# Kernel optimization log

Measured on AMD Instinct MI355X. Metric: run time of the kernel, lower is better.

The kernel has to match this reference:

```python
import jax, jax.numpy as jnp
import numpy as np

W_MAX, STEP, LEAK = 8, 1, 2
KSIZE = (W_MAX - 1) * (STEP + LEAK)  # 21
THETA = 40          # dense * w_max // 2 = 10*8//2
FODEP = KSIZE       # 21
PAD = KSIZE         # 21
NEURONS = 512


def make_w_kernel_table():
    # StepFireLeak response table, shape [w_max, KSIZE], time-flipped like torch .flip(1)
    w = np.arange(W_MAX, dtype=np.float64)[:, None]
    t = np.arange(KSIZE, dtype=np.float64)[None, :]
    w_step = np.maximum(np.floor(1.0 + t / STEP), 0.0)
    w_leak = np.maximum(np.ceil(w + ((w - 1.0) * STEP - t) / LEAK), 0.0)
    table = np.minimum(w_step, w_leak).astype(np.int32)[:, ::-1]
    return jnp.asarray(table)


def setup_inputs() -> dict:
    key = jax.random.key(0)
    k1, k2 = jax.random.split(key)
    B, C, S, T = 64, 1, 784, 500
    # sparse binary spike trains, p ~ 0.05
    input_spikes = (jax.random.randint(k1, (B, C, S, T), 0, 20) == 0).astype(jnp.float32)
    # learned integer synaptic weights in [0, w_max-1]
    weight = jax.random.randint(k2, (NEURONS, C * S), 0, W_MAX, dtype=jnp.int32)
    return {
        "input_spikes": input_spikes,
        "weight": weight,
        "w_kernel_table": make_w_kernel_table(),
    }


def reference(input_spikes, weight, w_kernel_table):
    B, C, S, T = input_spikes.shape
    x = input_spikes.reshape(B, C * S, T)
    # gather per-weight response kernel: [neurons, C*S, KSIZE]
    kernel = w_kernel_table[weight].astype(x.dtype)
    # cross-correlation, same semantics as torch conv1d (kernel already flipped)
    pot = jax.lax.conv_general_dilated(
        x, kernel, window_strides=(1,), padding=[(PAD, PAD)],
        dimension_numbers=("NCH", "OIH", "NCH"))
    pot = pot.reshape(B, 1, NEURONS, -1)            # [B, out_ch, neurons, Tp]
    pot_tfirst = jnp.moveaxis(pot, -1, 0)           # [Tp, B, ch, neurons]

    def step(depression, p_t):
        # p_t: [B, ch, neurons]
        winner = jnp.argmax(p_t, axis=-1)           # [B, ch]
        maxv = jnp.max(p_t, axis=-1)
        cond = (maxv > THETA) & (depression == 0)   # min_depression is all zeros
        winners_t = jax.nn.one_hot(winner, NEURONS, dtype=p_t.dtype) \
            * cond[..., None].astype(p_t.dtype)
        depression = jnp.maximum(0, depression + cond.astype(jnp.int32) * (FODEP + 1) - 1)
        return depression, winners_t

    dep0 = jnp.zeros((B, 1), jnp.int32)
    _, winners = jax.lax.scan(step, dep0, pot_tfirst)   # [Tp, B, ch, neurons]
    return jnp.moveaxis(winners, 0, -1)                 # [B, ch, neurons, Tp]
```

## Files before the change

kernel.cpp:

```cpp
#include <hip/hip_runtime.h>
#include <stdint.h>

#define NEURONS 512
#define SYN     784
#define TIN     500
#define TP      522
#define TPAD    528
#define BATCH   64
#define NCOL    (BATCH*TPAD)
#define XW2     18
#define NKK     98

typedef int i32x4 __attribute__((ext_vector_type(4)));

__global__ __launch_bounds__(256) void k_prep(
    const int* __restrict__ w, uint2* __restrict__ apk,
    const float* __restrict__ x, uint32_t* __restrict__ xbT,
    unsigned long long* __restrict__ partial)
{
    __shared__ unsigned char nib[16][128];
    const int bid = blockIdx.x, tid = threadIdx.x;
    if (bid < 1568) {
        int u = bid * 256 + tid;
        int half = u & 1, m = (u >> 1) & 15, quad = (u >> 5) & 3;
        int rowblk = (u >> 7) & 31, kk = u >> 12;
        int n = rowblk * 16 + m;
        int s = kk * 8 + quad * 2 + half;
        int wv = w[n * SYN + s];
        uint2 v;
        v.x = (wv < 4)  ? (1u << (8 * wv))       : 0u;
        v.y = (wv >= 4) ? (1u << (8 * (wv - 4))) : 0u;
        apk[u] = v;
        if (u < NCOL) partial[u] = 0ull;
    } else {
        int r0 = (bid - 1568) * 16;
        for (int e = tid; e < 2048; e += 256) {
            int row = e >> 7, q4 = e & 127;
            unsigned char v = 0;
            if (q4 < 125) {
                float4 f = *(const float4*)(x + (size_t)(r0 + row) * TIN + q4 * 4);
                v = (unsigned char)((f.x != 0.f) | ((f.y != 0.f) << 1) |
                                    ((f.z != 0.f) << 2) | ((f.w != 0.f) << 3));
            }
            nib[row][q4] = v;
        }
        __syncthreads();
        int row = tid >> 4, d = tid & 15;
        uint64_t u = *(const uint64_t*)&nib[row][d * 8];
        uint32_t wd = 0;
#pragma unroll
        for (int q = 0; q < 8; ++q)
            wd |= ((uint32_t)((u >> (8 * q)) & 0xFull)) << (4 * q);
        if (d == 15) wd &= 0xFFFFFu;
        int grow = r0 + row;
        int b = grow / SYN, s = grow - b * SYN;
        xbT[(size_t)(b * XW2 + 1 + d) * SYN + s] = wd;
        if (d == 0) {
            xbT[(size_t)(b * XW2) * SYN + s] = 0u;
            xbT[(size_t)(b * XW2 + 17) * SYN + s] = 0u;
        }
    }
}

__global__ __launch_bounds__(256) void k_bbuild(
    const uint32_t* __restrict__ xbT,
    const int*      __restrict__ wk,
    uint4*          __restrict__ Bg)
{
    __shared__ uint2 T0[2048];
    __shared__ uint2 T1[1024];
    __shared__ uint2 tapv[21];

    const int tid = threadIdx.x;
    if (tid < 21) {
        uint32_t lo = 0, hi = 0;
        for (int q = 0; q < 4; ++q) {
            lo |= ((uint32_t)wk[q * 21 + tid]) << (8 * q);
            hi |= ((uint32_t)wk[(q + 4) * 21 + tid]) << (8 * q);
        }
        tapv[tid] = make_uint2(lo, hi);
    }
    __syncthreads();
    for (int e = tid; e < 3072; e += 256) {
        int base_t = (e < 2048) ? 0 : 11;
        uint32_t mm = (e < 2048) ? e : (e - 2048);
        uint2 a = make_uint2(0u, 0u);
        while (mm) {
            int p = __builtin_ctz(mm);
            uint2 tv = tapv[base_t + p];
            a.x += tv.x; a.y += tv.y;
            mm &= mm - 1;
        }
        if (e < 2048) T0[e] = a; else T1[e - 2048] = a;
    }

    const int col = blockIdx.x * 64 + (tid >> 2);
    const int sp  = tid & 3;
    int b  = col / TPAD, t = col - b * TPAD;
    int bp = t + 11;
    const uint32_t xbase = (uint32_t)((b * XW2 + (bp >> 5)) * SYN + sp * 2);
    const uint32_t xsh   = (uint32_t)(bp & 31);
    __syncthreads();

    const int kk0 = blockIdx.y * 49, kk1 = kk0 + 49;
    for (int kk = kk0; kk < kk1; ++kk) {
        const uint2* px = (const uint2*)(xbT + xbase + kk * 8);
        uint2 lo = px[0];
        uint2 hi = px[SYN / 2];
        uint32_t w0 = __builtin_amdgcn_alignbit(hi.x, lo.x, xsh) & 0x1FFFFFu;
        uint32_t w1 = __builtin_amdgcn_alignbit(hi.y, lo.y, xsh) & 0x1FFFFFu;
        uint32_t l0 = w0 & 2047u, h0 = w0 >> 11;
        uint32_t l1 = w1 & 2047u, h1 = w1 >> 11;
        uint2 a0 = make_uint2(0u, 0u), a1 = make_uint2(0u, 0u);
        if (l0) { uint2 u = T0[l0]; a0.x += u.x; a0.y += u.y; }
        if (h0) { uint2 v = T1[h0]; a0.x += v.x; a0.y += v.y; }
        if (l1) { uint2 u = T0[l1]; a1.x += u.x; a1.y += u.y; }
        if (h1) { uint2 v = T1[h1]; a1.x += v.x; a1.y += v.y; }
        Bg[(size_t)(kk * NCOL + col) * 4 + sp] = make_uint4(a0.x, a0.y, a1.x, a1.y);
    }
}

__global__ __launch_bounds__(256, 4) void k_gemm2(
    const i32x4* __restrict__ Apk4,
    const i32x4* __restrict__ Bg4,
    unsigned long long* __restrict__ partial)
{
    __shared__ unsigned long long red[128 * 4];

    const int tid  = threadIdx.x;
    const int lane = tid & 63;
    const int wn   = tid >> 6;
    const int quad = lane >> 4, l15 = lane & 15;

    const int phys   = blockIdx.x;
    const int xcd    = phys & 7;
    const int jb     = phys >> 3;
    const int colblk = xcd * 33 + (jb >> 2);
    const int rowblk = jb & 3;

    const int m0   = rowblk * 128;
    const int col0 = colblk * 128;
    const int rb0  = rowblk * 8;
    const int cb   = col0 + wn * 32 + l15;

    const uint32_t pa0 = (uint32_t)(rb0 * 64 + lane);
    const uint32_t pb0 = (uint32_t)(cb * 4 + quad);

    i32x4 acc[8][2];
#pragma unroll
    for (int i = 0; i < 8; ++i)
#pragma unroll
        for (int jj = 0; jj < 2; ++jj) { i32x4 z = {0, 0, 0, 0}; acc[i][jj] = z; }

    for (int kk = 0; kk < NKK; ++kk) {
        i32x4 bf0 = Bg4[pb0 + (uint32_t)kk * (NCOL * 4)];
        i32x4 bf1 = Bg4[pb0 + (uint32_t)kk * (NCOL * 4) + 64];
        i32x4 af[8];
#pragma unroll
        for (int i = 0; i < 8; ++i)
            af[i] = Apk4[pa0 + (uint32_t)kk * 2048 + i * 64];
#pragma unroll
        for (int i = 0; i < 8; ++i) {
            acc[i][0] = __builtin_amdgcn_mfma_i32_16x16x64_i8(af[i], bf0, acc[i][0], 0, 0, 0);
            acc[i][1] = __builtin_amdgcn_mfma_i32_16x16x64_i8(af[i], bf1, acc[i][1], 0, 0, 0);
        }
    }

#pragma unroll
    for (int jj = 0; jj < 2; ++jj) {
        unsigned long long bp = 0ull;
#pragma unroll
        for (int i = 0; i < 8; ++i)
#pragma unroll
            for (int r = 0; r < 4; ++r) {
                int grow = m0 + i * 16 + quad * 4 + r;
                unsigned long long pk =
                    (((unsigned long long)(uint32_t)acc[i][jj][r]) << 32) |
                    (unsigned long long)(uint32_t)(511 - grow);
                bp = pk > bp ? pk : bp;
            }
        red[(wn * 32 + jj * 16 + l15) * 4 + quad] = bp;
    }
    __syncthreads();
    if (tid < 128) {
        unsigned long long b = red[tid * 4];
#pragma unroll
        for (int u = 1; u < 4; ++u) {
            unsigned long long v = red[tid * 4 + u];
            b = v > b ? v : b;
        }
        atomicMax(&partial[col0 + tid], b);
    }
}

__global__ __launch_bounds__(256) void k_firescan(
    const unsigned long long* __restrict__ partial, float* __restrict__ out)
{
    __shared__ int argL[576];
    __shared__ unsigned long long fm[9];
    const int b = blockIdx.x, tid = threadIdx.x;
    const int lane = tid & 63, wv = tid >> 6;

    float4* ob = (float4*)(out + (size_t)b * (NEURONS * TP));
    for (int i = tid; i < (NEURONS * TP) / 4; i += 256)
        ob[i] = make_float4(0.f, 0.f, 0.f, 0.f);

#pragma unroll
    for (int p = 0; p < 3; ++p) {
        int chunk = p * 4 + wv;
        if (chunk < 9) {
            int t = chunk * 64 + lane;
            int col = b * TPAD + (t < TPAD ? t : TPAD - 1);
            unsigned long long pv = partial[col];
            int best = (int)(pv >> 32);
            argL[t] = 511 - (int)(pv & 0xFFFFFFFFull);
            unsigned long long f = __ballot((t < TP) && (best > 40));
            if (lane == 0) fm[chunk] = f;
        }
    }
    __syncthreads();

    if (tid == 0) {
        unsigned short ts[26];
        int nf = 0, dep = 0;
        for (int c = 0; c < 9; ++c) {
            unsigned long long mm = fm[c];
            int pos = 0;
            while (pos < 64) {
                if (dep > 0) {
                    int adv = dep < (64 - pos) ? dep : (64 - pos);
                    dep -= adv; pos += adv; mm >>= adv;
                    continue;
                }
                if (mm == 0) break;
                int z = __builtin_ctzll(mm);
                pos += z; mm >>= z;
                ts[nf++] = (unsigned short)(c * 64 + pos);
                dep = 21; ++pos; mm >>= 1;
            }
        }
        for (int i = 0; i < nf; ++i) {
            int t = ts[i];
            out[(size_t)b * (NEURONS * TP) + (size_t)argL[t] * TP + t] = 1.0f;
        }
    }
}

__global__ __launch_bounds__(256) void k_gemm_fused(
    const i32x4*    __restrict__ Apk4,
    const uint32_t* __restrict__ xbT,
    const int*      __restrict__ wk,
    unsigned long long* __restrict__ partial)
{
    __shared__ uint2 T0[2048];
    __shared__ uint2 T1[1024];
    __shared__ unsigned long long red[128 * 4];
    __shared__ uint2 tapv[21];

    const int tid  = threadIdx.x;
    const int lane = tid & 63;
    const int wn   = tid >> 6;
    const int quad = lane >> 4, l15 = lane & 15;
    const int m0   = blockIdx.x * 128;
    const int col0 = blockIdx.y * 128;
    const int rb0  = blockIdx.x * 8;

    if (tid < 21) {
        uint32_t lo = 0, hi = 0;
        for (int q = 0; q < 4; ++q) {
            lo |= ((uint32_t)wk[q * 21 + tid]) << (8 * q);
            hi |= ((uint32_t)wk[(q + 4) * 21 + tid]) << (8 * q);
        }
        tapv[tid] = make_uint2(lo, hi);
    }
    __syncthreads();
    for (int e = tid; e < 3072; e += 256) {
        int base_t = (e < 2048) ? 0 : 11;
        uint32_t mm = (e < 2048) ? e : (e - 2048);
        uint2 a = make_uint2(0u, 0u);
        while (mm) {
            int p = __builtin_ctz(mm);
            uint2 tv = tapv[base_t + p];
            a.x += tv.x; a.y += tv.y;
            mm &= mm - 1;
        }
        if (e < 2048) T0[e] = a; else T1[e - 2048] = a;
    }

    uint32_t base[2]; uint32_t sh[2];
#pragma unroll
    for (int j = 0; j < 2; ++j) {
        int c = col0 + wn * 32 + j * 16 + l15;
        int b = c / TPAD, t = c - b * TPAD;
        int bp = t + 11;
        base[j] = (uint32_t)((b * XW2 + (bp >> 5)) * SYN + quad * 2);
        sh[j]   = (uint32_t)(bp & 31);
    }
    __syncthreads();

    i32x4 acc[8][2];
#pragma unroll
    for (int i = 0; i < 8; ++i)
#pragma unroll
        for (int j = 0; j < 2; ++j) { i32x4 z = {0, 0, 0, 0}; acc[i][j] = z; }

    for (int kk = 0; kk < NKK; ++kk) {
        i32x4 af[8];
#pragma unroll
        for (int i = 0; i < 8; ++i)
            af[i] = Apk4[(size_t)(kk * 32 + rb0 + i) * 64 + lane];
        i32x4 bf[2];
#pragma unroll
        for (int j = 0; j < 2; ++j) {
            const uint2* px = (const uint2*)(xbT + base[j] + kk * 8);
            uint2 lo = px[0];
            uint2 hi = px[SYN / 2];
            uint32_t win0 = __builtin_amdgcn_alignbit(hi.x, lo.x, sh[j]) & 0x1FFFFFu;
            uint32_t win1 = __builtin_amdgcn_alignbit(hi.y, lo.y, sh[j]) & 0x1FFFFFu;
            uint2 u0 = T0[win0 & 2047], v0 = T1[win0 >> 11];
            uint2 u1 = T0[win1 & 2047], v1 = T1[win1 >> 11];
            i32x4 bb;
            bb[0] = (int)(u0.x + v0.x); bb[1] = (int)(u0.y + v0.y);
            bb[2] = (int)(u1.x + v1.x); bb[3] = (int)(u1.y + v1.y);
            bf[j] = bb;
        }
#pragma unroll
        for (int i = 0; i < 8; ++i)
#pragma unroll
            for (int j = 0; j < 2; ++j)
                acc[i][j] = __builtin_amdgcn_mfma_i32_16x16x64_i8(af[i], bf[j], acc[i][j], 0, 0, 0);
    }

#pragma unroll
    for (int j = 0; j < 2; ++j) {
        unsigned long long bp = 0ull;
#pragma unroll
        for (int i = 0; i < 8; ++i)
#pragma unroll
            for (int r = 0; r < 4; ++r) {
                int grow = m0 + i * 16 + quad * 4 + r;
                unsigned long long pk =
                    (((unsigned long long)(uint32_t)acc[i][j][r]) << 32) |
                    (unsigned long long)(uint32_t)(511 - grow);
                bp = pk > bp ? pk : bp;
            }
        red[(wn * 32 + j * 16 + l15) * 4 + quad] = bp;
    }
    __syncthreads();
    if (tid < 128) {
        unsigned long long b = red[tid * 4];
#pragma unroll
        for (int u = 1; u < 4; ++u) {
            unsigned long long v = red[tid * 4 + u];
            b = v > b ? v : b;
        }
        atomicMax(&partial[col0 + tid], b);
    }
}

__global__ void k_fire(const unsigned long long* __restrict__ partial,
                       int* __restrict__ argT, unsigned long long* __restrict__ fireM) {
    int id   = blockIdx.x * 4 + (threadIdx.x >> 6);
    int lane = threadIdx.x & 63;
    int b    = id / 9, ch = id - b * 9;
    int t    = ch * 64 + lane;
    int col  = b * TPAD + (t < TPAD ? t : TPAD - 1);
    unsigned long long pv = partial[col];
    int best = (int)(pv >> 32);
    int arg  = 511 - (int)(pv & 0xFFFFFFFFull);
    argT[id * 64 + lane] = arg;
    unsigned long long f = __ballot((t < TP) && (best > 40));
    if (lane == 0) fireM[id] = f;
}

__global__ void k_scan(const unsigned long long* __restrict__ fireM,
                       const int* __restrict__ argT, float* __restrict__ out) {
    int b = threadIdx.x;
    unsigned long long fm[9];
#pragma unroll
    for (int c = 0; c < 9; ++c) fm[c] = fireM[b * 9 + c];
    unsigned short ts[26];
    int nf = 0, dep = 0;
    for (int c = 0; c < 9; ++c) {
        unsigned long long mm = fm[c];
        int pos = 0;
        while (pos < 64) {
            if (dep > 0) {
                int adv = dep < (64 - pos) ? dep : (64 - pos);
                dep -= adv; pos += adv; mm >>= adv;
                continue;
            }
            if (mm == 0) break;
            int z = __builtin_ctzll(mm);
            pos += z; mm >>= z;
            ts[nf++] = (unsigned short)(c * 64 + pos);
            dep = 21; ++pos; mm >>= 1;
        }
    }
    for (int i = 0; i < nf; ++i) {
        int t = ts[i];
        int a = argT[(b * 9 + (t >> 6)) * 64 + (t & 63)];
        out[(size_t)b * (NEURONS * TP) + (size_t)a * TP + t] = 1.0f;
    }
}

extern "C" void kernel_launch(void* const* d_in, const int* in_sizes, int n_in,
                              void* d_out, int out_size, void* d_ws, size_t ws_size,
                              hipStream_t stream) {
    const float* x      = (const float*)d_in[0];
    const int*   weight = (const int*)d_in[1];
    const int*   wk     = (const int*)d_in[2];

    char* ws = (char*)d_ws;
    uint2*              Apk     = (uint2*)(ws);
    uint32_t*           xbT     = (uint32_t*)(ws + 3211264);
    unsigned long long* partial = (unsigned long long*)(ws + 6823936);
    int*                argT    = (int*)(ws + 7094272);
    unsigned long long* fireM   = (unsigned long long*)(ws + 7241728);
    uint4*              Bg      = (uint4*)(ws + 7246336);
    const size_t WS_SPLIT_NEED = 7246336ull + 211746816ull;

    float* out = (float*)d_out;

    if (ws_size >= WS_SPLIT_NEED) {
        k_prep<<<4704, 256, 0, stream>>>(weight, Apk, x, xbT, partial);
        k_bbuild<<<dim3(528, 2), 256, 0, stream>>>(xbT, wk, Bg);
        k_gemm2<<<1056, 256, 0, stream>>>((const i32x4*)Apk, (const i32x4*)Bg, partial);
        k_firescan<<<BATCH, 256, 0, stream>>>(partial, out);
    } else {
        hipMemsetAsync(out, 0, (size_t)out_size * 4, stream);
        hipMemsetAsync(partial, 0, NCOL * 8, stream);
        k_prep<<<4704, 256, 0, stream>>>(weight, Apk, x, xbT, partial);
        k_gemm_fused<<<dim3(4, NCOL / 128), 256, 0, stream>>>((const i32x4*)Apk, xbT, wk, partial);
        k_fire<<<144, 256, 0, stream>>>(partial, argT, fireM);
        k_scan<<<1, 64, 0, stream>>>(fireM, argT, out);
    }
}
```

Baseline: 403.0 us.

## Fuse prep, GEMM with on-the-fly B build, and fire scan into one cooperative kernel

Replaces the four-kernel pipeline with a single persistent cooperative kernel that uses grid syncs between phases. The GEMM now builds B fragments on the fly from the bit-packed spike table and LDS lookup tables, instead of staging a large precomputed B matrix in global memory. The output zeroing moves from the fire-scan phase into the prep phase. Together these remove launch overhead and the large B write and re-read. The cost is extra ALU and LDS work inside the GEMM loop, grid-sync latency, and possible occupancy limits from the larger combined shared-memory footprint.

Measured after the change: 702.7 us. +74.4%, slower.

```diff
diff --git a/kernel.cpp b/kernel.cpp
--- a/kernel.cpp
+++ b/kernel.cpp
@@ -1,5 +1,8 @@
 #include <hip/hip_runtime.h>
+#include <hip/hip_cooperative_groups.h>
 #include <stdint.h>
+
+namespace cg = cooperative_groups;
 
 #define NEURONS 512
 #define SYN     784
@@ -10,13 +13,241 @@
 #define NCOL    (BATCH*TPAD)
 #define XW2     18
 #define NKK     98
+#define OUTF4   ((BATCH*NEURONS*TP)/4)
 
 typedef int i32x4 __attribute__((ext_vector_type(4)));
+
+__global__ __launch_bounds__(256, 4) void k_all(
+    const int* __restrict__ w, uint2* __restrict__ apk,
+    const float* __restrict__ x, uint32_t* __restrict__ xbT,
+    unsigned long long* __restrict__ partial, float* __restrict__ out,
+    const int* __restrict__ wk)
+{
+    __shared__ unsigned char nib[16][128];
+    __shared__ uint2 T0[2048];
+    __shared__ uint2 T1[1024];
+    __shared__ unsigned long long red[128 * 4];
+    __shared__ uint2 tapv[21];
+    __shared__ int argL[576];
+    __shared__ unsigned long long fm[9];
+
+    cg::grid_group grid = cg::this_grid();
+    const int tid = threadIdx.x;
+
+    for (int vb = blockIdx.x; vb < 5216; vb += gridDim.x) {
+        if (vb < 1568) {
+            int u = vb * 256 + tid;
+            int half = u & 1, m = (u >> 1) & 15, quad = (u >> 5) & 3;
+            int rowblk = (u >> 7) & 31, kk = u >> 12;
+            int n = rowblk * 16 + m;
+            int s = kk * 8 + quad * 2 + half;
+            int wv = w[n * SYN + s];
+            uint2 v;
+            v.x = (wv < 4)  ? (1u << (8 * wv))       : 0u;
+            v.y = (wv >= 4) ? (1u << (8 * (wv - 4))) : 0u;
+            apk[u] = v;
+            if (u < NCOL) partial[u] = 0ull;
+        } else if (vb < 4704) {
+            int r0 = (vb - 1568) * 16;
+            __syncthreads();
+            for (int e = tid; e < 2048; e += 256) {
+                int row = e >> 7, q4 = e & 127;
+                unsigned char v = 0;
+                if (q4 < 125) {
+                    float4 f = *(const float4*)(x + (size_t)(r0 + row) * TIN + q4 * 4);
+                    v = (unsigned char)((f.x != 0.f) | ((f.y != 0.f) << 1) |
+                                        ((f.z != 0.f) << 2) | ((f.w != 0.f) << 3));
+                }
+                nib[row][q4] = v;
+            }
+            __syncthreads();
+            int row = tid >> 4, d = tid & 15;
+            uint64_t u = *(const uint64_t*)&nib[row][d * 8];
+            uint32_t wd = 0;
+#pragma unroll
+            for (int q = 0; q < 8; ++q)
+                wd |= ((uint32_t)((u >> (8 * q)) & 0xFull)) << (4 * q);
+            if (d == 15) wd &= 0xFFFFFu;
+            int grow = r0 + row;
+            int b = grow / SYN, s = grow - b * SYN;
+            xbT[(size_t)(b * XW2 + 1 + d) * SYN + s] = wd;
+            if (d == 0) {
+                xbT[(size_t)(b * XW2) * SYN + s] = 0u;
+                xbT[(size_t)(b * XW2 + 17) * SYN + s] = 0u;
+            }
+        } else {
+            const float4 z = make_float4(0.f, 0.f, 0.f, 0.f);
+            float4* out4 = (float4*)out;
+            for (size_t i = (size_t)(vb - 4704) * 256 + tid; i < OUTF4; i += 512 * 256)
+                out4[i] = z;
+        }
+    }
+    grid.sync();
+
+    const int lane = tid & 63;
+    const int wn   = tid >> 6;
+    const int quad = lane >> 4, l15 = lane & 15;
+
+    if (tid < 21) {
+        uint32_t lo = 0, hi = 0;
+        for (int q = 0; q < 4; ++q) {
+            lo |= ((uint32_t)wk[q * 21 + tid]) << (8 * q);
+            hi |= ((uint32_t)wk[(q + 4) * 21 + tid]) << (8 * q);
+        }
+        tapv[tid] = make_uint2(lo, hi);
+    }
+    __syncthreads();
+    for (int e = tid; e < 3072; e += 256) {
+        int base_t = (e < 2048) ? 0 : 11;
+        uint32_t mm = (e < 2048) ? e : (e - 2048);
+        uint2 a = make_uint2(0u, 0u);
+        while (mm) {
+            int p = __builtin_ctz(mm);
+            uint2 tv = tapv[base_t + p];
+            a.x += tv.x; a.y += tv.y;
+            mm &= mm - 1;
+        }
+        if (e < 2048) T0[e] = a; else T1[e - 2048] = a;
+    }
+    __syncthreads();
+
+    for (int vb = blockIdx.x; vb < 1056; vb += gridDim.x) {
+        const int xcd    = vb & 7;
+        const int jb     = vb >> 3;
+        const int colblk = xcd * 33 + (jb >> 2);
+        const int rowblk = jb & 3;
+
+        const int m0   = rowblk * 128;
+        const int col0 = colblk * 128;
+        const int rb0  = rowblk * 8;
+
+        uint32_t base[2]; uint32_t sh[2];
+#pragma unroll
+        for (int j = 0; j < 2; ++j) {
+            int c = col0 + wn * 32 + j * 16 + l15;
+            int b = c / TPAD, t = c - b * TPAD;
+            int bp = t + 11;
+            base[j] = (uint32_t)((b * XW2 + (bp >> 5)) * SYN + quad * 2);
+            sh[j]   = (uint32_t)(bp & 31);
+        }
+        const uint32_t pa0 = (uint32_t)(rb0 * 64 + lane);
+
+        i32x4 acc[8][2];
+#pragma unroll
+        for (int i = 0; i < 8; ++i)
+#pragma unroll
+            for (int j = 0; j < 2; ++j) { i32x4 z = {0, 0, 0, 0}; acc[i][j] = z; }
+
+        const i32x4* Apk4 = (const i32x4*)apk;
+        for (int kk = 0; kk < NKK; ++kk) {
+            i32x4 af[8];
+#pragma unroll
+            for (int i = 0; i < 8; ++i)
+                af[i] = Apk4[pa0 + (uint32_t)kk * 2048 + i * 64];
+            i32x4 bf[2];
+#pragma unroll
+            for (int j = 0; j < 2; ++j) {
+                const uint2* px = (const uint2*)(xbT + base[j] + kk * 8);
+                uint2 lo = px[0];
+                uint2 hi = px[SYN / 2];
+                uint32_t win0 = __builtin_amdgcn_alignbit(hi.x, lo.x, sh[j]) & 0x1FFFFFu;
+                uint32_t win1 = __builtin_amdgcn_alignbit(hi.y, lo.y, sh[j]) & 0x1FFFFFu;
+                uint32_t l0 = win0 & 2047u, h0 = win0 >> 11;
+                uint32_t l1 = win1 & 2047u, h1 = win1 >> 11;
+                uint2 a0 = make_uint2(0u, 0u), a1 = make_uint2(0u, 0u);
+                if (l0) { uint2 u = T0[l0]; a0.x += u.x; a0.y += u.y; }
+                if (h0) { uint2 v = T1[h0]; a0.x += v.x; a0.y += v.y; }
+                if (l1) { uint2 u = T0[l1]; a1.x += u.x; a1.y += u.y; }
+                if (h1) { uint2 v = T1[h1]; a1.x += v.x; a1.y += v.y; }
+                i32x4 bb;
+                bb[0] = (int)a0.x; bb[1] = (int)a0.y;
+                bb[2] = (int)a1.x; bb[3] = (int)a1.y;
+                bf[j] = bb;
+            }
+#pragma unroll
+            for (int i = 0; i < 8; ++i)
+#pragma unroll
+                for (int j = 0; j < 2; ++j)
+                    acc[i][j] = __builtin_amdgcn_mfma_i32_16x16x64_i8(af[i], bf[j], acc[i][j], 0, 0, 0);
+        }
+
+#pragma unroll
+        for (int j = 0; j < 2; ++j) {
+            unsigned long long bp = 0ull;
+#pragma unroll
+            for (int i = 0; i < 8; ++i)
+#pragma unroll
+                for (int r = 0; r < 4; ++r) {
+                    int grow = m0 + i * 16 + quad * 4 + r;
+                    unsigned long long pk =
+                        (((unsigned long long)(uint32_t)acc[i][j][r]) << 32) |
+                        (unsigned long long)(uint32_t)(511 - grow);
+                    bp = pk > bp ? pk : bp;
+                }
+            red[(wn * 32 + j * 16 + l15) * 4 + quad] = bp;
+        }
+        __syncthreads();
+        if (tid < 128) {
+            unsigned long long b = red[tid * 4];
+#pragma unroll
+            for (int u = 1; u < 4; ++u) {
+                unsigned long long v = red[tid * 4 + u];
+                b = v > b ? v : b;
+            }
+            atomicMax(&partial[col0 + tid], b);
+        }
+        __syncthreads();
+    }
+    grid.sync();
+
+    if (blockIdx.x < BATCH) {
+        const int b = blockIdx.x;
+        const int wv = tid >> 6;
+#pragma unroll
+        for (int p = 0; p < 3; ++p) {
+            int chunk = p * 4 + wv;
+            if (chunk < 9) {
+                int t = chunk * 64 + lane;
+                int col = b * TPAD + (t < TPAD ? t : TPAD - 1);
+                unsigned long long pv = partial[col];
+                int best = (int)(pv >> 32);
+                argL[t] = 511 - (int)(pv & 0xFFFFFFFFull);
+                unsigned long long f = __ballot((t < TP) && (best > 40));
+                if (lane == 0) fm[chunk] = f;
+            }
+        }
+        __syncthreads();
+        if (tid == 0) {
+            unsigned short ts[26];
+            int nf = 0, dep = 0;
+            for (int c = 0; c < 9; ++c) {
+                unsigned long long mm = fm[c];
+                int pos = 0;
+                while (pos < 64) {
+                    if (dep > 0) {
+                        int adv = dep < (64 - pos) ? dep : (64 - pos);
+                        dep -= adv; pos += adv; mm >>= adv;
+                        continue;
+                    }
+                    if (mm == 0) break;
+                    int z = __builtin_ctzll(mm);
+                    pos += z; mm >>= z;
+                    ts[nf++] = (unsigned short)(c * 64 + pos);
+                    dep = 21; ++pos; mm >>= 1;
+                }
+            }
+            for (int i = 0; i < nf; ++i) {
+                int t = ts[i];
+                out[(size_t)b * (NEURONS * TP) + (size_t)argL[t] * TP + t] = 1.0f;
+            }
+        }
+    }
+}
 
 __global__ __launch_bounds__(256) void k_prep(
     const int* __restrict__ w, uint2* __restrict__ apk,
     const float* __restrict__ x, uint32_t* __restrict__ xbT,
-    unsigned long long* __restrict__ partial)
+    unsigned long long* __restrict__ partial, float4* __restrict__ out4)
 {
     __shared__ unsigned char nib[16][128];
     const int bid = blockIdx.x, tid = threadIdx.x;
@@ -32,7 +263,7 @@
         v.y = (wv >= 4) ? (1u << (8 * (wv - 4))) : 0u;
         apk[u] = v;
         if (u < NCOL) partial[u] = 0ull;
-    } else {
+    } else if (bid < 4704) {
         int r0 = (bid - 1568) * 16;
         for (int e = tid; e < 2048; e += 256) {
             int row = e >> 7, q4 = e & 127;
@@ -59,19 +290,39 @@
             xbT[(size_t)(b * XW2) * SYN + s] = 0u;
             xbT[(size_t)(b * XW2 + 17) * SYN + s] = 0u;
         }
+    } else {
+        const float4 z = make_float4(0.f, 0.f, 0.f, 0.f);
+        for (size_t i = (size_t)(bid - 4704) * 256 + tid; i < OUTF4; i += 512 * 256)
+            out4[i] = z;
     }
 }
 
-__global__ __launch_bounds__(256) void k_bbuild(
+__global__ __launch_bounds__(256, 4) void k_gemm_fused2(
+    const i32x4*    __restrict__ Apk4,
     const uint32_t* __restrict__ xbT,
     const int*      __restrict__ wk,
-    uint4*          __restrict__ Bg)
+    unsigned long long* __restrict__ partial)
 {
     __shared__ uint2 T0[2048];
     __shared__ uint2 T1[1024];
+    __shared__ unsigned long long red[128 * 4];
     __shared__ uint2 tapv[21];
 
-    const int tid = threadIdx.x;
+    const int tid  = threadIdx.x;
+    const int lane = tid & 63;
+    const int wn   = tid >> 6;
+    const int quad = lane >> 4, l15 = lane & 15;
+
+    const int phys   = blockIdx.x;
+    const int xcd    = phys & 7;
+    const int jb     = phys >> 3;
+    const int colblk = xcd * 33 + (jb >> 2);
+    const int rowblk = jb & 3;
+
+    const int m0   = rowblk * 128;
+    const int col0 = colblk * 128;
+    const int rb0  = rowblk * 8;
+
     if (tid < 21) {
         uint32_t lo = 0, hi = 0;
         for (int q = 0; q < 4; ++q) {
@@ -94,80 +345,59 @@
         if (e < 2048) T0[e] = a; else T1[e - 2048] = a;
     }
 
-    const int col = blockIdx.x * 64 + (tid >> 2);
-    const int sp  = tid & 3;
-    int b  = col / TPAD, t = col - b * TPAD;
-    int bp = t + 11;
-    const uint32_t xbase = (uint32_t)((b * XW2 + (bp >> 5)) * SYN + sp * 2);
-    const uint32_t xsh   = (uint32_t)(bp & 31);
+    uint32_t base[2]; uint32_t sh[2];
+#pragma unroll
+    for (int j = 0; j < 2; ++j) {
+        int c = col0 + wn * 32 + j * 16 + l15;
+        int b = c / TPAD, t = c - b * TPAD;
+        int bp = t + 11;
+        base[j] = (uint32_t)((b * XW2 + (bp >> 5)) * SYN + quad * 2);
+        sh[j]   = (uint32_t)(bp & 31);
+    }
     __syncthreads();
 
-    const int kk0 = blockIdx.y * 49, kk1 = kk0 + 49;
-    for (int kk = kk0; kk < kk1; ++kk) {
-        const uint2* px = (const uint2*)(xbT + xbase + kk * 8);
-        uint2 lo = px[0];
-        uint2 hi = px[SYN / 2];
-        uint32_t w0 = __builtin_amdgcn_alignbit(hi.x, lo.x, xsh) & 0x1FFFFFu;
-        uint32_t w1 = __builtin_amdgcn_alignbit(hi.y, lo.y, xsh) & 0x1FFFFFu;
-        uint32_t l0 = w0 & 2047u, h0 = w0 >> 11;
-        uint32_t l1 = w1 & 2047u, h1 = w1 >> 11;
-        uint2 a0 = make_uint2(0u, 0u), a1 = make_uint2(0u, 0u);
-        if (l0) { uint2 u = T0[l0]; a0.x += u.x; a0.y += u.y; }
-        if (h0) { uint2 v = T1[h0]; a0.x += v.x; a0.y += v.y; }
-        if (l1) { uint2 u = T0[l1]; a1.x += u.x; a1.y += u.y; }
-        if (h1) { uint2 v = T1[h1]; a1.x += v.x; a1.y += v.y; }
-        Bg[(size_t)(kk * NCOL + col) * 4 + sp] = make_uint4(a0.x, a0.y, a1.x, a1.y);
-    }
-}
-
-__global__ __launch_bounds__(256, 4) void k_gemm2(
-    const i32x4* __restrict__ Apk4,
-    const i32x4* __restrict__ Bg4,
-    unsigned long long* __restrict__ partial)
-{
-    __shared__ unsigned long long red[128 * 4];
-
-    const int tid  = threadIdx.x;
-    const int lane = tid & 63;
-    const int wn   = tid >> 6;
-    const int quad = lane >> 4, l15 = lane & 15;
-
-    const int phys   = blockIdx.x;
-    const int xcd    = phys & 7;
-    const int jb     = phys >> 3;
-    const int colblk = xcd * 33 + (jb >> 2);
-    const int rowblk = jb & 3;
-
-    const int m0   = rowblk * 128;
-    const int col0 = colblk * 128;
-    const int rb0  = rowblk * 8;
-    const int cb   = col0 + wn * 32 + l15;
-
     const uint32_t pa0 = (uint32_t)(rb0 * 64 + lane);
-    const uint32_t pb0 = (uint32_t)(cb * 4 + quad);
 
     i32x4 acc[8][2];
 #pragma unroll
     for (int i = 0; i < 8; ++i)
 #pragma unroll
-        for (int jj = 0; jj < 2; ++jj) { i32x4 z = {0, 0, 0, 0}; acc[i][jj] = z; }
+        for (int j = 0; j < 2; ++j) { i32x4 z = {0, 0, 0, 0}; acc[i][j] = z; }
 
     for (int kk = 0; kk < NKK; ++kk) {
-        i32x4 bf0 = Bg4[pb0 + (uint32_t)kk * (NCOL * 4)];
-        i32x4 bf1 = Bg4[pb0 + (uint32_t)kk * (NCOL * 4) + 64];
         i32x4 af[8];
 #pragma unroll
         for (int i = 0; i < 8; ++i)
             af[i] = Apk4[pa0 + (uint32_t)kk * 2048 + i * 64];
-#pragma unroll
-        for (int i = 0; i < 8; ++i) {
-            acc[i][0] = __builtin_amdgcn_mfma_i32_16x16x64_i8(af[i], bf0, acc[i][0], 0, 0, 0);
-            acc[i][1] = __builtin_amdgcn_mfma_i32_16x16x64_i8(af[i], bf1, acc[i][1], 0, 0, 0);
-        }
-    }
-
-#pragma unroll
-    for (int jj = 0; jj < 2; ++jj) {
+        i32x4 bf[2];
+#pragma unroll
+        for (int j = 0; j < 2; ++j) {
+            const uint2* px = (const uint2*)(xbT + base[j] + kk * 8);
+            uint2 lo = px[0];
+            uint2 hi = px[SYN / 2];
+            uint32_t win0 = __builtin_amdgcn_alignbit(hi.x, lo.x, sh[j]) & 0x1FFFFFu;
+            uint32_t win1 = __builtin_amdgcn_alignbit(hi.y, lo.y, sh[j]) & 0x1FFFFFu;
+            uint32_t l0 = win0 & 2047u, h0 = win0 >> 11;
+            uint32_t l1 = win1 & 2047u, h1 = win1 >> 11;
+            uint2 a0 = make_uint2(0u, 0u), a1 = make_uint2(0u, 0u);
+            if (l0) { uint2 u = T0[l0]; a0.x += u.x; a0.y += u.y; }
+            if (h0) { uint2 v = T1[h0]; a0.x += v.x; a0.y += v.y; }
+            if (l1) { uint2 u = T0[l1]; a1.x += u.x; a1.y += u.y; }
+            if (h1) { uint2 v = T1[h1]; a1.x += v.x; a1.y += v.y; }
+            i32x4 bb;
+            bb[0] = (int)a0.x; bb[1] = (int)a0.y;
+            bb[2] = (int)a1.x; bb[3] = (int)a1.y;
+            bf[j] = bb;
+        }
+#pragma unroll
+        for (int i = 0; i < 8; ++i)
+#pragma unroll
+            for (int j = 0; j < 2; ++j)
+                acc[i][j] = __builtin_amdgcn_mfma_i32_16x16x64_i8(af[i], bf[j], acc[i][j], 0, 0, 0);
+    }
+
+#pragma unroll
+    for (int j = 0; j < 2; ++j) {
         unsigned long long bp = 0ull;
 #pragma unroll
         for (int i = 0; i < 8; ++i)
@@ -175,11 +405,11 @@
             for (int r = 0; r < 4; ++r) {
                 int grow = m0 + i * 16 + quad * 4 + r;
                 unsigned long long pk =
-                    (((unsigned long long)(uint32_t)acc[i][jj][r]) << 32) |
+                    (((unsigned long long)(uint32_t)acc[i][j][r]) << 32) |
                     (unsigned long long)(uint32_t)(511 - grow);
                 bp = pk > bp ? pk : bp;
             }
-        red[(wn * 32 + jj * 16 + l15) * 4 + quad] = bp;
+        red[(wn * 32 + j * 16 + l15) * 4 + quad] = bp;
     }
     __syncthreads();
     if (tid < 128) {
@@ -200,10 +430,6 @@
     __shared__ unsigned long long fm[9];
     const int b = blockIdx.x, tid = threadIdx.x;
     const int lane = tid & 63, wv = tid >> 6;
-
-    float4* ob = (float4*)(out + (size_t)b * (NEURONS * TP));
-    for (int i = tid; i < (NEURONS * TP) / 4; i += 256)
-        ob[i] = make_float4(0.f, 0.f, 0.f, 0.f);
 
 #pragma unroll
     for (int p = 0; p < 3; ++p) {
@@ -246,164 +472,6 @@
     }
 }
 
-__global__ __launch_bounds__(256) void k_gemm_fused(
-    const i32x4*    __restrict__ Apk4,
-    const uint32_t* __restrict__ xbT,
-    const int*      __restrict__ wk,
-    unsigned long long* __restrict__ partial)
-{
-    __shared__ uint2 T0[2048];
-    __shared__ uint2 T1[1024];
-    __shared__ unsigned long long red[128 * 4];
-    __shared__ uint2 tapv[21];
-
-    const int tid  = threadIdx.x;
-    const int lane = tid & 63;
-    const int wn   = tid >> 6;
-    const int quad = lane >> 4, l15 = lane & 15;
-    const int m0   = blockIdx.x * 128;
-    const int col0 = blockIdx.y * 128;
-    const int rb0  = blockIdx.x * 8;
-
-    if (tid < 21) {
-        uint32_t lo = 0, hi = 0;
-        for (int q = 0; q < 4; ++q) {
-            lo |= ((uint32_t)wk[q * 21 + tid]) << (8 * q);
-            hi |= ((uint32_t)wk[(q + 4) * 21 + tid]) << (8 * q);
-        }
-        tapv[tid] = make_uint2(lo, hi);
-    }
-    __syncthreads();
-    for (int e = tid; e < 3072; e += 256) {
-        int base_t = (e < 2048) ? 0 : 11;
-        uint32_t mm = (e < 2048) ? e : (e - 2048);
-        uint2 a = make_uint2(0u, 0u);
-        while (mm) {
-            int p = __builtin_ctz(mm);
-            uint2 tv = tapv[base_t + p];
-            a.x += tv.x; a.y += tv.y;
-            mm &= mm - 1;
-        }
-        if (e < 2048) T0[e] = a; else T1[e - 2048] = a;
-    }
-
-    uint32_t base[2]; uint32_t sh[2];
-#pragma unroll
-    for (int j = 0; j < 2; ++j) {
-        int c = col0 + wn * 32 + j * 16 + l15;
-        int b = c / TPAD, t = c - b * TPAD;
-        int bp = t + 11;
-        base[j] = (uint32_t)((b * XW2 + (bp >> 5)) * SYN + quad * 2);
-        sh[j]   = (uint32_t)(bp & 31);
-    }
-    __syncthreads();
-
-    i32x4 acc[8][2];
-#pragma unroll
-    for (int i = 0; i < 8; ++i)
-#pragma unroll
-        for (int j = 0; j < 2; ++j) { i32x4 z = {0, 0, 0, 0}; acc[i][j] = z; }
-
-    for (int kk = 0; kk < NKK; ++kk) {
-        i32x4 af[8];
-#pragma unroll
-        for (int i = 0; i < 8; ++i)
-            af[i] = Apk4[(size_t)(kk * 32 + rb0 + i) * 64 + lane];
-        i32x4 bf[2];
-#pragma unroll
-        for (int j = 0; j < 2; ++j) {
-            const uint2* px = (const uint2*)(xbT + base[j] + kk * 8);
-            uint2 lo = px[0];
-            uint2 hi = px[SYN / 2];
-            uint32_t win0 = __builtin_amdgcn_alignbit(hi.x, lo.x, sh[j]) & 0x1FFFFFu;
-            uint32_t win1 = __builtin_amdgcn_alignbit(hi.y, lo.y, sh[j]) & 0x1FFFFFu;
-            uint2 u0 = T0[win0 & 2047], v0 = T1[win0 >> 11];
-            uint2 u1 = T0[win1 & 2047], v1 = T1[win1 >> 11];
-            i32x4 bb;
-            bb[0] = (int)(u0.x + v0.x); bb[1] = (int)(u0.y + v0.y);
-            bb[2] = (int)(u1.x + v1.x); bb[3] = (int)(u1.y + v1.y);
-            bf[j] = bb;
-        }
-#pragma unroll
-        for (int i = 0; i < 8; ++i)
-#pragma unroll
-            for (int j = 0; j < 2; ++j)
-                acc[i][j] = __builtin_amdgcn_mfma_i32_16x16x64_i8(af[i], bf[j], acc[i][j], 0, 0, 0);
-    }
-
-#pragma unroll
-    for (int j = 0; j < 2; ++j) {
-        unsigned long long bp = 0ull;
-#pragma unroll
-        for (int i = 0; i < 8; ++i)
-#pragma unroll
-            for (int r = 0; r < 4; ++r) {
-                int grow = m0 + i * 16 + quad * 4 + r;
-                unsigned long long pk =
-                    (((unsigned long long)(uint32_t)acc[i][j][r]) << 32) |
-                    (unsigned long long)(uint32_t)(511 - grow);
-                bp = pk > bp ? pk : bp;
-            }
-        red[(wn * 32 + j * 16 + l15) * 4 + quad] = bp;
-    }
-    __syncthreads();
-    if (tid < 128) {
-        unsigned long long b = red[tid * 4];
-#pragma unroll
-        for (int u = 1; u < 4; ++u) {
-            unsigned long long v = red[tid * 4 + u];
-            b = v > b ? v : b;
-        }
-        atomicMax(&partial[col0 + tid], b);
-    }
-}
-
-__global__ void k_fire(const unsigned long long* __restrict__ partial,
-                       int* __restrict__ argT, unsigned long long* __restrict__ fireM) {
-    int id   = blockIdx.x * 4 + (threadIdx.x >> 6);
-    int lane = threadIdx.x & 63;
-    int b    = id / 9, ch = id - b * 9;
-    int t    = ch * 64 + lane;
-    int col  = b * TPAD + (t < TPAD ? t : TPAD - 1);
-    unsigned long long pv = partial[col];
-    int best = (int)(pv >> 32);
-    int arg  = 511 - (int)(pv & 0xFFFFFFFFull);
-    argT[id * 64 + lane] = arg;
-    unsigned long long f = __ballot((t < TP) && (best > 40));
-    if (lane == 0) fireM[id] = f;
-}
-
-__global__ void k_scan(const unsigned long long* __restrict__ fireM,
-                       const int* __restrict__ argT, float* __restrict__ out) {
-    int b = threadIdx.x;
-    unsigned long long fm[9];
-#pragma unroll
-    for (int c = 0; c < 9; ++c) fm[c] = fireM[b * 9 + c];
-    unsigned short ts[26];
-    int nf = 0, dep = 0;
-    for (int c = 0; c < 9; ++c) {
-        unsigned long long mm = fm[c];
-        int pos = 0;
-        while (pos < 64) {
-            if (dep > 0) {
-                int adv = dep < (64 - pos) ? dep : (64 - pos);
-                dep -= adv; pos += adv; mm >>= adv;
-                continue;
-            }
-            if (mm == 0) break;
-            int z = __builtin_ctzll(mm);
-            pos += z; mm >>= z;
-            ts[nf++] = (unsigned short)(c * 64 + pos);
-            dep = 21; ++pos; mm >>= 1;
-        }
-    }
-    for (int i = 0; i < nf; ++i) {
-        int t = ts[i];
-        int a = argT[(b * 9 + (t >> 6)) * 64 + (t & 63)];
-        out[(size_t)b * (NEURONS * TP) + (size_t)a * TP + t] = 1.0f;
-    }
-}
-
 extern "C" void kernel_launch(void* const* d_in, const int* in_sizes, int n_in,
                               void* d_out, int out_size, void* d_ws, size_t ws_size,
                               hipStream_t stream) {
@@ -415,24 +483,19 @@
     uint2*              Apk     = (uint2*)(ws);
     uint32_t*           xbT     = (uint32_t*)(ws + 3211264);
     unsigned long long* partial = (unsigned long long*)(ws + 6823936);
-    int*                argT    = (int*)(ws + 7094272);
-    unsigned long long* fireM   = (unsigned long long*)(ws + 7241728);
-    uint4*              Bg      = (uint4*)(ws + 7246336);
-    const size_t WS_SPLIT_NEED = 7246336ull + 211746816ull;
 
     float* out = (float*)d_out;
 
-    if (ws_size >= WS_SPLIT_NEED) {
-        k_prep<<<4704, 256, 0, stream>>>(weight, Apk, x, xbT, partial);
-        k_bbuild<<<dim3(528, 2), 256, 0, stream>>>(xbT, wk, Bg);
-        k_gemm2<<<1056, 256, 0, stream>>>((const i32x4*)Apk, (const i32x4*)Bg, partial);
+    const int* w_a = weight; uint2* apk_a = Apk; const float* x_a = x;
+    uint32_t* xbT_a = xbT; unsigned long long* p_a = partial;
+    float* out_a = out; const int* wk_a = wk;
+    void* kargs[] = { (void*)&w_a, (void*)&apk_a, (void*)&x_a, (void*)&xbT_a,
+                      (void*)&p_a, (void*)&out_a, (void*)&wk_a };
+    hipError_t e = hipLaunchCooperativeKernel((const void*)k_all, dim3(1024),
+                                              dim3(256), kargs, 0, stream);
+    if (e != hipSuccess) {
+        k_prep<<<5216, 256, 0, stream>>>(weight, Apk, x, xbT, partial, (float4*)out);
+        k_gemm_fused2<<<1056, 256, 0, stream>>>((const i32x4*)Apk, xbT, wk, partial);
         k_firescan<<<BATCH, 256, 0, stream>>>(partial, out);
-    } else {
-        hipMemsetAsync(out, 0, (size_t)out_size * 4, stream);
-        hipMemsetAsync(partial, 0, NCOL * 8, stream);
-        k_prep<<<4704, 256, 0, stream>>>(weight, Apk, x, xbT, partial);
-        k_gemm_fused<<<dim3(4, NCOL / 128), 256, 0, stream>>>((const i32x4*)Apk, xbT, wk, partial);
-        k_fire<<<144, 256, 0, stream>>>(partial, argT, fireM);
-        k_scan<<<1, 64, 0, stream>>>(fireM, argT, out);
     }
 }
```
